# Optimization experiments

Hardware: AMD Instinct MI355X
Metric: run time of the kernel (lower is better)

The kernel has to match this reference:

```python
import jax, jax.numpy as jnp
import numpy as np

K_LAYERS = 2   # top-k layers kept in zeta routing
K_EXPERTS = 2  # top-k experts kept in alpha routing


def _topk_sparse_softmax(logits, k):
    """Keep top-k along last axis, set rest to -inf, softmax. logits [..., N]."""
    lead = logits.shape[:-1]
    n = logits.shape[-1]
    flat = logits.reshape(-1, n)
    vals, idx = jax.lax.top_k(flat, k)                      # [R,k]
    sparse = jnp.full_like(flat, -jnp.inf)
    rows = jnp.arange(flat.shape[0])[:, None]
    sparse = sparse.at[rows, idx].set(vals)
    return jax.nn.softmax(sparse, axis=-1).reshape(*lead, n)


def _lora_layer(h, W, b, A, B, zeta_l, alpha_l):
    """One backbone Linear + gated LoRA expert mixture + ReLU.
    h [B,in], W [out,in], A [E,r,in], B [E,out,r], zeta_l [B], alpha_l [B,E].
    """
    lin = h @ W.T + b                                       # [B,out]
    t = jnp.einsum('bi,eri->ber', h, A)                     # [B,E,r]
    tw = t * alpha_l[:, :, None]                            # weight experts early
    lora_sum = jnp.einsum('ber,eor->bo', tw, B)             # [B,out]
    return jax.nn.relu(lin + zeta_l[:, None] * lora_sum)


def _routing(domain_ids, dom_emb, layer_pos, Wi1, bi1, Wi2, bi2,
             Wa1, ba1, Wa2, ba2, gate_logits, R_benefit):
    M, H = dom_emb.shape
    L = layer_pos.shape[0]
    router_inp = jnp.concatenate([
        jnp.broadcast_to(dom_emb[:, None, :], (M, L, H)),
        jnp.broadcast_to(layer_pos[None, :, :], (M, L, H)),
    ], axis=-1)                                             # [M,L,2H]
    hz = jax.nn.relu(router_inp @ Wi1.T + bi1)
    zeta_logits = (hz @ Wi2.T + bi2)[..., 0]                # [M,L]
    zeta_all = _topk_sparse_softmax(zeta_logits, K_LAYERS)
    ha = jax.nn.relu(router_inp @ Wa1.T + ba1)
    alpha_logits = ha @ Wa2.T + ba2                         # [M,L,E]
    alpha_all = _topk_sparse_softmax(alpha_logits, K_EXPERTS)
    # gated benefit matrix, row-normalized
    R = jax.nn.softplus(gate_logits) * R_benefit
    R = R / jnp.clip(R.sum(-1, keepdims=True), 1e-12)
    zeta_agg = R @ zeta_all                                 # [M,L]
    alpha_agg = jnp.einsum('mn,nle->mle', R, alpha_all)     # [M,L,E]
    return zeta_agg[domain_ids], alpha_agg[domain_ids]      # [B,L],[B,L,E]


def setup_inputs() -> dict:
    key = jax.random.key(0)
    ks = jax.random.split(key, 32)
    Bsz, D0, D1, D2, D3 = 16384, 2048, 2048, 1024, 512
    E, r, M, H, L = 4, 8, 8, 64, 3
    s = 0.02
    return {
        'x': jax.random.normal(ks[0], (Bsz, D0), jnp.float32),
        'domain_ids': jax.random.randint(ks[1], (Bsz,), 0, M),
        'W1': jax.random.normal(ks[2], (D1, D0)) * s, 'b1': jnp.zeros((D1,)),
        'W2': jax.random.normal(ks[3], (D2, D1)) * s, 'b2': jnp.zeros((D2,)),
        'W3': jax.random.normal(ks[4], (D3, D2)) * s, 'b3': jnp.zeros((D3,)),
        'A1': jax.random.normal(ks[5], (E, r, D0)) * s, 'B1': jax.random.normal(ks[6], (E, D1, r)) * s,
        'A2': jax.random.normal(ks[7], (E, r, D1)) * s, 'B2': jax.random.normal(ks[8], (E, D2, r)) * s,
        'A3': jax.random.normal(ks[9], (E, r, D2)) * s, 'B3': jax.random.normal(ks[10], (E, D3, r)) * s,
        'dom_emb': jax.random.normal(ks[11], (M, H)) * s,
        'layer_pos': jax.random.normal(ks[12], (L, H)) * s,
        'Wi1': jax.random.normal(ks[13], (H, 2 * H)) * 0.1, 'bi1': jnp.zeros((H,)),
        'Wi2': jax.random.normal(ks[14], (1, H)) * 0.1, 'bi2': jnp.zeros((1,)),
        'Wa1': jax.random.normal(ks[15], (H, 2 * H)) * 0.1, 'ba1': jnp.zeros((H,)),
        'Wa2': jax.random.normal(ks[16], (E, H)) * 0.1, 'ba2': jnp.zeros((E,)),
        'gate_logits': jax.random.normal(ks[17], (M, M)) * 0.1,
        'R_benefit': jax.random.uniform(ks[18], (M, M)),
    }


def reference(x, domain_ids, W1, b1, W2, b2, W3, b3,
              A1, B1, A2, B2, A3, B3,
              dom_emb, layer_pos, Wi1, bi1, Wi2, bi2,
              Wa1, ba1, Wa2, ba2, gate_logits, R_benefit):
    zeta, alpha = _routing(domain_ids, dom_emb, layer_pos, Wi1, bi1, Wi2, bi2,
                           Wa1, ba1, Wa2, ba2, gate_logits, R_benefit)
    h = _lora_layer(x, W1, b1, A1, B1, zeta[:, 0], alpha[:, 0])
    h = _lora_layer(h, W2, b2, A2, B2, zeta[:, 1], alpha[:, 1])
    h = _lora_layer(h, W3, b3, A3, B3, zeta[:, 2], alpha[:, 2])
    return h
```

## Files before the change

### kernel.cpp

```cpp
#include <hip/hip_runtime.h>

typedef __bf16 bf16_t;
typedef __bf16 bf16x8 __attribute__((ext_vector_type(8)));
typedef __bf16 bf16x4_v __attribute__((ext_vector_type(4)));
typedef float f32x4 __attribute__((ext_vector_type(4)));

#define AS1 __attribute__((address_space(1)))
#define AS3 __attribute__((address_space(3)))

__device__ __forceinline__ void gload_lds16(const void* g, void* l) {
    __builtin_amdgcn_global_load_lds((AS1 void*)(void*)g, (AS3 void*)l, 16, 0, 0);
}

__global__ void routing_kernel(
    const float* __restrict__ dom_emb, const float* __restrict__ layer_pos,
    const float* __restrict__ Wi1, const float* __restrict__ bi1,
    const float* __restrict__ Wi2, const float* __restrict__ bi2,
    const float* __restrict__ Wa1, const float* __restrict__ ba1,
    const float* __restrict__ Wa2, const float* __restrict__ ba2,
    const float* __restrict__ gate_logits, const float* __restrict__ R_benefit,
    float* __restrict__ salpha)
{
    constexpr int M = 8, L = 3, E = 4, H = 64;
    __shared__ float zl[M * L];
    __shared__ float al[M * L][E];
    __shared__ float zeta_all[M][L];
    __shared__ float alpha_all[M][L][E];
    const int t = threadIdx.x;
    const int ml = t >> 3, js = t & 7;
    if (ml < M * L) {
        const int m = ml / L, l = ml % L;
        float zacc = 0.f;
        float aacc[E] = {0.f, 0.f, 0.f, 0.f};
        for (int jj = 0; jj < 8; ++jj) {
            const int j = js * 8 + jj;
            float hz = bi1[j], ha = ba1[j];
            for (int i = 0; i < H; ++i) {
                const float de = dom_emb[m * H + i];
                const float lp = layer_pos[l * H + i];
                hz += de * Wi1[j * 2 * H + i] + lp * Wi1[j * 2 * H + H + i];
                ha += de * Wa1[j * 2 * H + i] + lp * Wa1[j * 2 * H + H + i];
            }
            hz = fmaxf(hz, 0.f); ha = fmaxf(ha, 0.f);
            zacc += hz * Wi2[j];
            for (int e = 0; e < E; ++e) aacc[e] += ha * Wa2[e * H + j];
        }
        #pragma unroll
        for (int off = 4; off >= 1; off >>= 1) {
            zacc += __shfl_down(zacc, off, 8);
            for (int e = 0; e < E; ++e) aacc[e] += __shfl_down(aacc[e], off, 8);
        }
        if (js == 0) {
            zl[ml] = zacc + bi2[0];
            for (int e = 0; e < E; ++e) al[ml][e] = aacc[e] + ba2[e];
        }
    }
    __syncthreads();
    if (t < M) {
        const int m = t;
        float v[3] = { zl[m * L + 0], zl[m * L + 1], zl[m * L + 2] };
        int di = 0; float dv = v[0];
        for (int i = 1; i < 3; ++i) if (v[i] <= dv) { dv = v[i]; di = i; }
        float mx = -1e30f;
        for (int i = 0; i < 3; ++i) if (i != di) mx = fmaxf(mx, v[i]);
        float s = 0.f, ev[3];
        for (int i = 0; i < 3; ++i) { ev[i] = (i == di) ? 0.f : expf(v[i] - mx); s += ev[i]; }
        for (int i = 0; i < 3; ++i) zeta_all[m][i] = ev[i] / s;
        for (int l = 0; l < L; ++l) {
            float a[4];
            for (int e = 0; e < 4; ++e) a[e] = al[m * L + l][e];
            int i1 = 0;
            for (int e = 1; e < 4; ++e) if (a[e] > a[i1]) i1 = e;
            int i2 = -1;
            for (int e = 0; e < 4; ++e) { if (e == i1) continue; if (i2 < 0 || a[e] > a[i2]) i2 = e; }
            const float mx2 = fmaxf(a[i1], a[i2]);
            const float e1 = expf(a[i1] - mx2), e2 = expf(a[i2] - mx2);
            const float ss = e1 + e2;
            for (int e = 0; e < 4; ++e) alpha_all[m][l][e] = 0.f;
            alpha_all[m][l][i1] = e1 / ss;
            alpha_all[m][l][i2] = e2 / ss;
        }
    }
    __syncthreads();
    if (t < M) {
        const int m = t;
        float Rrow[8]; float rs = 0.f;
        for (int n = 0; n < M; ++n) {
            const float g = gate_logits[m * M + n];
            const float rr = log1pf(expf(g)) * R_benefit[m * M + n];
            Rrow[n] = rr; rs += rr;
        }
        rs = fmaxf(rs, 1e-12f);
        for (int l = 0; l < L; ++l) {
            float zag = 0.f, aag[4] = {0.f, 0.f, 0.f, 0.f};
            for (int n = 0; n < M; ++n) {
                const float w = Rrow[n] / rs;
                zag += w * zeta_all[n][l];
                for (int e = 0; e < 4; ++e) aag[e] += w * alpha_all[n][l][e];
            }
            for (int e = 0; e < 4; ++e) salpha[(m * L + l) * 4 + e] = zag * aag[e];
        }
    }
}

__global__ void cvt_f32_bf16(const float* __restrict__ in, bf16_t* __restrict__ out, const int n4) {
    const int i = blockIdx.x * 256 + threadIdx.x;
    if (i < n4) {
        const float4 v = ((const float4*)in)[i];
        bf16x4_v o;
        o[0] = (__bf16)v.x; o[1] = (__bf16)v.y; o[2] = (__bf16)v.z; o[3] = (__bf16)v.w;
        ((bf16x4_v*)out)[i] = o;
    }
}

__global__ void bepi_cvt(const float* __restrict__ Bsrc, bf16_t* __restrict__ out, const int Dout) {
    const int idx = blockIdx.x * 256 + threadIdx.x;
    if (idx < Dout * 32) {
        const int o = idx >> 5, c = idx & 31, e = c >> 3, r = c & 7;
        out[idx] = (__bf16)Bsrc[((size_t)e * Dout + o) * 8 + r];
    }
}

template<bool F32IN>
__global__ void __launch_bounds__(256) tw_kernel(
    const void* __restrict__ hin, bf16_t* __restrict__ xb_out,
    const bf16_t* __restrict__ Acat, const float* __restrict__ salpha,
    const int* __restrict__ dom, const int layer, const int K,
    bf16_t* __restrict__ TWb)
{
    const int t = threadIdx.x, wid = t >> 6, lane = t & 63;
    const int rb = blockIdx.x * 64 + wid * 16;
    const int ln15 = lane & 15, kg = (lane >> 4) * 8;
    const int row = rb + ln15;
    f32x4 acc0 = {0.f, 0.f, 0.f, 0.f}, acc1 = {0.f, 0.f, 0.f, 0.f};
    const bf16_t* pa0 = Acat + (size_t)ln15 * K + kg;
    const bf16_t* pa1 = pa0 + (size_t)16 * K;
    for (int k0 = 0; k0 < K; k0 += 32) {
        bf16x8 a;
        if constexpr (F32IN) {
            const float* px = (const float*)hin + (size_t)row * K + k0 + kg;
            const float4 x0 = *(const float4*)px;
            const float4 x1 = *(const float4*)(px + 4);
            a[0] = (__bf16)x0.x; a[1] = (__bf16)x0.y; a[2] = (__bf16)x0.z; a[3] = (__bf16)x0.w;
            a[4] = (__bf16)x1.x; a[5] = (__bf16)x1.y; a[6] = (__bf16)x1.z; a[7] = (__bf16)x1.w;
            *(bf16x8*)(xb_out + (size_t)row * K + k0 + kg) = a;
        } else {
            a = *(const bf16x8*)((const bf16_t*)hin + (size_t)row * K + k0 + kg);
        }
        const bf16x8 b0 = *(const bf16x8*)(pa0 + k0);
        const bf16x8 b1 = *(const bf16x8*)(pa1 + k0);
        acc0 = __builtin_amdgcn_mfma_f32_16x16x32_bf16(a, b0, acc0, 0, 0, 0);
        acc1 = __builtin_amdgcn_mfma_f32_16x16x32_bf16(a, b1, acc1, 0, 0, 0);
    }
    const int rbase = rb + (lane >> 4) * 4;
    #pragma unroll
    for (int i = 0; i < 4; ++i) {
        const int r2 = rbase + i;
        const int d = dom[r2];
        const float* sa = salpha + (d * 3 + layer) * 4;
        const float s0 = sa[ln15 >> 3];
        const float s1 = sa[2 + (ln15 >> 3)];
        TWb[(size_t)r2 * 32 + ln15]      = (__bf16)(acc0[i] * s0);
        TWb[(size_t)r2 * 32 + 16 + ln15] = (__bf16)(acc1[i] * s1);
    }
}


__device__ __forceinline__ void stage_chunk64(const bf16_t* g, int ldK, char* chunk, int t) {
    #pragma unroll
    for (int w = 0; w < 2; ++w) {
        const int row = t >> 2;
        const int sl = t & 3;
        const int src = sl ^ (((row >> 3) & 1) << 1);
        gload_lds16(g + (size_t)row * ldK + w * 32 + src * 8, chunk + w * 8192 + t * 16);
    }
}

__device__ __forceinline__ void stage_chunk32(const bf16_t* g, char* chunk, int t) {
    const int row = t >> 2;
    const int sl = t & 3;
    const int src = sl ^ (((row >> 3) & 1) << 1);
    gload_lds16(g + (size_t)row * 32 + src * 8, chunk + t * 16);
}

__global__ void __launch_bounds__(512, 2) gemm_lora8(
    const bf16_t* __restrict__ Abuf, const bf16_t* __restrict__ Wbuf,
    const float* __restrict__ bias, const bf16_t* __restrict__ TWb,
    const bf16_t* __restrict__ Bepi, bf16_t* __restrict__ outp,
    const int N, const int K, const int nwg_n)
{
    __shared__ __align__(1024) char lds[131072];
    const int t = threadIdx.x;
    const int wid = t >> 6, lane = t & 63;
    const int wm = wid >> 2, wn = wid & 3, wnh = wn >> 1;
    const int cpx = gridDim.x >> 3;
    const int wg = (blockIdx.x & 7) * cpx + (blockIdx.x >> 3);
    const int row0 = (wg / nwg_n) * 256, col0 = (wg % nwg_n) * 256;

    const int r15 = lane & 15;
    const int swb = ((lane >> 4) ^ (((lane >> 3) & 1) << 1)) << 4;

    auto achunk = [&](int p, int c) -> char* { return lds + (((p << 1) + c) << 14); };
    auto bchunk = [&](int p, int c) -> char* { return lds + 65536 + (((p << 1) + c) << 14); };

    const bf16_t* Ab = Abuf + (size_t)row0 * K;
    const bf16_t* Bb = Wbuf + (size_t)col0 * K;
    const size_t halfA = (size_t)128 * K;

    f32x4 acc[8][4] = {};
    bf16x8 aF[4], bF[4];

    auto readA = [&](char* c, int mbase, int kq) {
        #pragma unroll
        for (int i = 0; i < 4; ++i)
            aF[i] = *(const bf16x8*)(c + (kq << 13) + (((mbase + i) * 16 + r15) << 6) + swb);
    };
    auto readB = [&](char* c, int kq) {
        #pragma unroll
        for (int nf = 0; nf < 4; ++nf)
            bF[nf] = *(const bf16x8*)(c + (kq << 13) + (((wn & 1) * 64 + nf * 16 + r15) << 6) + swb);
    };
    auto mfma16 = [&](int mbase) {
        __builtin_amdgcn_s_setprio(1);
        #pragma unroll
        for (int mf = 0; mf < 4; ++mf)
            #pragma unroll
            for (int nf = 0; nf < 4; ++nf)
                acc[mbase + mf][nf] =
                    __builtin_amdgcn_mfma_f32_16x16x32_bf16(aF[mf], bF[nf], acc[mbase + mf][nf], 0, 0, 0);
        __builtin_amdgcn_s_setprio(0);
    };
    #define MIDSYNC() do { __builtin_amdgcn_s_barrier(); \
        asm volatile("s_waitcnt lgkmcnt(0)" ::: "memory"); \
        __builtin_amdgcn_sched_barrier(0); } while (0)
    #define ENDBAR() __builtin_amdgcn_s_barrier()

    const int NT = K >> 6;

    stage_chunk64(Ab,               K, achunk(0, 0), t);
    stage_chunk64(Ab + halfA,       K, achunk(0, 1), t);
    stage_chunk64(Bb,               K, bchunk(0, 0), t);
    stage_chunk64(Bb + halfA,       K, bchunk(0, 1), t);
    stage_chunk64(Bb + 64,          K, bchunk(1, 0), t);
    stage_chunk64(Bb + halfA + 64,  K, bchunk(1, 1), t);
    asm volatile("s_waitcnt vmcnt(4)" ::: "memory");
    __builtin_amdgcn_s_barrier();

    for (int T = 0; T < NT; ++T) {
        const int p = T & 1, q = p ^ 1;
        const size_t ko1 = (size_t)(T + 1) << 6, ko2 = (size_t)(T + 2) << 6;
        char* myA = achunk(p, wm);
        char* myB = bchunk(p, wnh);
        if (T + 1 < NT) stage_chunk64(Ab + ko1, K, achunk(q, 0), t);
        readA(myA, 0, 0);
        readB(myB, 0);
        if (T == NT - 1) asm volatile("s_waitcnt vmcnt(0)" ::: "memory");
        MIDSYNC();
        mfma16(0);
        ENDBAR();
        if (T + 1 < NT) stage_chunk64(Ab + halfA + ko1, K, achunk(q, 1), t);
        readA(myA, 4, 0);
        MIDSYNC();
        mfma16(4);
        ENDBAR();
        readA(myA, 4, 1);
        readB(myB, 1);
        MIDSYNC();
        mfma16(4);
        ENDBAR();
        if (T + 2 < NT) {
            stage_chunk64(Bb + ko2,         K, bchunk(p, 0), t);
            stage_chunk64(Bb + halfA + ko2, K, bchunk(p, 1), t);
        }
        readA(myA, 0, 1);
        asm volatile("s_waitcnt vmcnt(4)" ::: "memory");
        MIDSYNC();
        mfma16(0);
        ENDBAR();
    }

    {
        const int q2 = NT & 1;
        stage_chunk32(TWb + (size_t)row0 * 32,          achunk(q2, 0), t);
        stage_chunk32(TWb + (size_t)(row0 + 128) * 32,  achunk(q2, 1), t);
        stage_chunk32(Bepi + (size_t)col0 * 32,         bchunk(q2, 0), t);
        stage_chunk32(Bepi + (size_t)(col0 + 128) * 32, bchunk(q2, 1), t);
        asm volatile("s_waitcnt vmcnt(0)" ::: "memory");
        __builtin_amdgcn_s_barrier();
        char* lA_ = achunk(q2, wm);
        char* lB_ = bchunk(q2, wnh);
        #pragma unroll
        for (int nf = 0; nf < 4; ++nf)
            bF[nf] = *(const bf16x8*)(lB_ + (((wn & 1) * 64 + nf * 16 + r15) << 6) + swb);
        #pragma unroll
        for (int i = 0; i < 4; ++i)
            aF[i] = *(const bf16x8*)(lA_ + ((i * 16 + r15) << 6) + swb);
        asm volatile("s_waitcnt lgkmcnt(0)" ::: "memory");
        __builtin_amdgcn_sched_barrier(0);
        mfma16(0);
        #pragma unroll
        for (int i = 0; i < 4; ++i)
            aF[i] = *(const bf16x8*)(lA_ + (((i + 4) * 16 + r15) << 6) + swb);
        asm volatile("s_waitcnt lgkmcnt(0)" ::: "memory");
        __builtin_amdgcn_sched_barrier(0);
        mfma16(4);
    }

    const int orow = row0 + wm * 128 + (lane >> 4) * 4;
    const int ocol = col0 + wn * 64 + r15;
    #pragma unroll
    for (int nf = 0; nf < 4; ++nf) {
        const int col = ocol + nf * 16;
        const float bn = bias[col];
        #pragma unroll
        for (int mf = 0; mf < 8; ++mf) {
            const int rbase = orow + mf * 16;
            #pragma unroll
            for (int i = 0; i < 4; ++i) {
                const float v = fmaxf(acc[mf][nf][i] + bn, 0.f);
                outp[(size_t)(rbase + i) * N + col] = (__bf16)v;
            }
        }
    }
    #undef MIDSYNC
    #undef ENDBAR
}

#define BM 128
#define BN 128
#define BK 32

template<bool OUT_F32>
__global__ void __launch_bounds__(256) gemm_lora(
    const bf16_t* __restrict__ Abuf, const bf16_t* __restrict__ Wbuf,
    const float* __restrict__ bias, const bf16_t* __restrict__ TWb,
    const bf16_t* __restrict__ Bepi, void* __restrict__ outp,
    const int N, const int K)
{
    __shared__ bf16_t lA[BM * BK];
    __shared__ bf16_t lB[BN * BK];
    const int t = threadIdx.x;
    const int row0 = blockIdx.y * BM;
    const int col0 = blockIdx.x * BN;
    const int wid = t >> 6, lane = t & 63;
    const int wr = wid >> 1, wc = wid & 1;
    const int ln15 = lane & 15, kg = (lane >> 4) * 8;
    const int srow = t >> 2, sg8 = (t & 3) * 8;
    const bf16_t* gA = Abuf + (size_t)(row0 + srow) * K + sg8;
    const bf16_t* gB = Wbuf + (size_t)(col0 + srow) * K + sg8;
    bf16_t* ldA  = &lA[t * 8];
    bf16_t* ldA2 = &lA[2048 + t * 8];
    bf16_t* ldB  = &lB[t * 8];
    bf16_t* ldB2 = &lB[2048 + t * 8];
    f32x4 acc[4][4] = {};
    const int aoff = (wr * 64 + ln15) * BK + kg;
    const int boff = (wc * 64 + ln15) * BK + kg;

    auto compute_tile = [&]() {
        bf16x8 af[4], bfr[4];
        #pragma unroll
        for (int m = 0; m < 4; ++m) af[m] = *(const bf16x8*)&lA[aoff + m * 16 * BK];
        #pragma unroll
        for (int n = 0; n < 4; ++n) bfr[n] = *(const bf16x8*)&lB[boff + n * 16 * BK];
        #pragma unroll
        for (int m = 0; m < 4; ++m)
            #pragma unroll
            for (int n = 0; n < 4; ++n)
                acc[m][n] = __builtin_amdgcn_mfma_f32_16x16x32_bf16(af[m], bfr[n], acc[m][n], 0, 0, 0);
    };

    const size_t half = (size_t)64 * K;
    const int nk = K / BK;
    for (int kt = 0; kt < nk; ++kt) {
        gload_lds16(gA + kt * BK, ldA);
        gload_lds16(gA + half + kt * BK, ldA2);
        gload_lds16(gB + kt * BK, ldB);
        gload_lds16(gB + half + kt * BK, ldB2);
        __syncthreads();
        compute_tile();
        __syncthreads();
    }
    gload_lds16(TWb + (size_t)(row0 + srow) * 32 + sg8, ldA);
    gload_lds16(TWb + (size_t)(row0 + 64 + srow) * 32 + sg8, ldA2);
    gload_lds16(Bepi + (size_t)(col0 + srow) * 32 + sg8, ldB);
    gload_lds16(Bepi + (size_t)(col0 + 64 + srow) * 32 + sg8, ldB2);
    __syncthreads();
    compute_tile();

    const int orow = row0 + wr * 64 + (lane >> 4) * 4;
    const int ocol = col0 + wc * 64 + ln15;
    #pragma unroll
    for (int n = 0; n < 4; ++n) {
        const int col = ocol + n * 16;
        const float bn = bias[col];
        #pragma unroll
        for (int m = 0; m < 4; ++m) {
            const int rbase = orow + m * 16;
            #pragma unroll
            for (int i = 0; i < 4; ++i) {
                const float v = fmaxf(acc[m][n][i] + bn, 0.f);
                if constexpr (OUT_F32)
                    ((float*)outp)[(size_t)(rbase + i) * N + col] = v;
                else
                    ((bf16_t*)outp)[(size_t)(rbase + i) * N + col] = (__bf16)v;
            }
        }
    }
}

extern "C" void kernel_launch(void* const* d_in, const int* in_sizes, int n_in,
                              void* d_out, int out_size, void* d_ws, size_t ws_size,
                              hipStream_t stream)
{
    const float* x    = (const float*)d_in[0];
    const int*   dom  = (const int*)d_in[1];
    const float* W1   = (const float*)d_in[2];  const float* b1  = (const float*)d_in[3];
    const float* W2   = (const float*)d_in[4];  const float* b2  = (const float*)d_in[5];
    const float* W3   = (const float*)d_in[6];  const float* b3  = (const float*)d_in[7];
    const float* A1   = (const float*)d_in[8];  const float* B1  = (const float*)d_in[9];
    const float* A2   = (const float*)d_in[10]; const float* B2  = (const float*)d_in[11];
    const float* A3   = (const float*)d_in[12]; const float* B3  = (const float*)d_in[13];
    const float* dome = (const float*)d_in[14]; const float* lpos = (const float*)d_in[15];
    const float* Wi1  = (const float*)d_in[16]; const float* bi1 = (const float*)d_in[17];
    const float* Wi2  = (const float*)d_in[18]; const float* bi2 = (const float*)d_in[19];
    const float* Wa1  = (const float*)d_in[20]; const float* ba1 = (const float*)d_in[21];
    const float* Wa2  = (const float*)d_in[22]; const float* ba2 = (const float*)d_in[23];
    const float* gate = (const float*)d_in[24]; const float* Rb  = (const float*)d_in[25];
    (void)in_sizes; (void)n_in; (void)out_size; (void)ws_size;

    constexpr int Bsz = 16384, D0 = 2048, D1 = 2048, D2 = 1024, D3 = 512;

    char* ws = (char*)d_ws;
    size_t off = 0;
    auto alloc = [&](size_t bytes) -> void* {
        void* p = ws + off;
        off = (off + bytes + 255) & ~(size_t)255;
        return p;
    };
    float*  salpha = (float*) alloc(8 * 3 * 4 * sizeof(float));
    bf16_t* W1b = (bf16_t*)alloc((size_t)D1 * D0 * 2);
    bf16_t* W2b = (bf16_t*)alloc((size_t)D2 * D1 * 2);
    bf16_t* W3b = (bf16_t*)alloc((size_t)D3 * D2 * 2);
    bf16_t* Ac1 = (bf16_t*)alloc((size_t)32 * D0 * 2);
    bf16_t* Ac2 = (bf16_t*)alloc((size_t)32 * D1 * 2);
    bf16_t* Ac3 = (bf16_t*)alloc((size_t)32 * D2 * 2);
    bf16_t* Be1 = (bf16_t*)alloc((size_t)D1 * 32 * 2);
    bf16_t* Be2 = (bf16_t*)alloc((size_t)D2 * 32 * 2);
    bf16_t* Be3 = (bf16_t*)alloc((size_t)D3 * 32 * 2);
    bf16_t* TWb = (bf16_t*)alloc((size_t)Bsz * 32 * 2);
    bf16_t* xb  = (bf16_t*)alloc((size_t)Bsz * D0 * 2);
    bf16_t* h1b = (bf16_t*)alloc((size_t)Bsz * D1 * 2);
    bf16_t* h2b = xb;

    routing_kernel<<<1, 256, 0, stream>>>(dome, lpos, Wi1, bi1, Wi2, bi2,
                                          Wa1, ba1, Wa2, ba2, gate, Rb, salpha);

    cvt_f32_bf16<<<(D1 * D0 / 4 + 255) / 256, 256, 0, stream>>>(W1, W1b, D1 * D0 / 4);
    cvt_f32_bf16<<<(D2 * D1 / 4 + 255) / 256, 256, 0, stream>>>(W2, W2b, D2 * D1 / 4);
    cvt_f32_bf16<<<(D3 * D2 / 4 + 255) / 256, 256, 0, stream>>>(W3, W3b, D3 * D2 / 4);
    cvt_f32_bf16<<<(32 * D0 / 4 + 255) / 256, 256, 0, stream>>>(A1, Ac1, 32 * D0 / 4);
    cvt_f32_bf16<<<(32 * D1 / 4 + 255) / 256, 256, 0, stream>>>(A2, Ac2, 32 * D1 / 4);
    cvt_f32_bf16<<<(32 * D2 / 4 + 255) / 256, 256, 0, stream>>>(A3, Ac3, 32 * D2 / 4);
    bepi_cvt<<<(D1 * 32 + 255) / 256, 256, 0, stream>>>(B1, Be1, D1);
    bepi_cvt<<<(D2 * 32 + 255) / 256, 256, 0, stream>>>(B2, Be2, D2);
    bepi_cvt<<<(D3 * 32 + 255) / 256, 256, 0, stream>>>(B3, Be3, D3);

    tw_kernel<true><<<Bsz / 64, 256, 0, stream>>>(x, xb, Ac1, salpha, dom, 0, D0, TWb);
    gemm_lora8<<<(Bsz / 256) * (D1 / 256), 512, 0, stream>>>(xb, W1b, b1, TWb, Be1, h1b, D1, D0, D1 / 256);
    tw_kernel<false><<<Bsz / 64, 256, 0, stream>>>(h1b, nullptr, Ac2, salpha, dom, 1, D1, TWb);
    gemm_lora8<<<(Bsz / 256) * (D2 / 256), 512, 0, stream>>>(h1b, W2b, b2, TWb, Be2, h2b, D2, D1, D2 / 256);
    tw_kernel<false><<<Bsz / 64, 256, 0, stream>>>(h2b, nullptr, Ac3, salpha, dom, 2, D2, TWb);
    gemm_lora<true><<<dim3(D3 / BN, Bsz / BM), 256, 0, stream>>>(h2b, W3b, b3, TWb, Be3, d_out, D3, D2);
}
```

Measured before the change: 418.3 us.

## Interleave GEMM tile prefetch per phase and fuse weight conversion launches

The main GEMM's global-to-LDS staging is reorganized. Instead of loading whole 64-wide A and B chunks at a few points, with B prefetched two tiles ahead, it now issues half-chunk loads for the next tile spread across the four MFMA phases. It uses precomputed per-thread source pointers and tuned vmcnt waits, so load issue should overlap compute more evenly with less address arithmetic. Separately, the nine small f32-to-bf16 conversion launches are merged into two kernels that write one contiguous destination. That merge assumes the bf16 buffers are allocated back-to-back and hardcodes the problem sizes.

```diff
diff --git a/kernel.cpp b/kernel.cpp
--- a/kernel.cpp
+++ b/kernel.cpp
@@ -103,22 +103,44 @@
     }
 }
 
-__global__ void cvt_f32_bf16(const float* __restrict__ in, bf16_t* __restrict__ out, const int n4) {
+__global__ void cvt_fused(const float* __restrict__ s0, const float* __restrict__ s1,
+                          const float* __restrict__ s2, const float* __restrict__ s3,
+                          const float* __restrict__ s4, const float* __restrict__ s5,
+                          bf16_t* __restrict__ dst)
+{
     const int i = blockIdx.x * 256 + threadIdx.x;
-    if (i < n4) {
-        const float4 v = ((const float4*)in)[i];
-        bf16x4_v o;
-        o[0] = (__bf16)v.x; o[1] = (__bf16)v.y; o[2] = (__bf16)v.z; o[3] = (__bf16)v.w;
-        ((bf16x4_v*)out)[i] = o;
-    }
-}
-
-__global__ void bepi_cvt(const float* __restrict__ Bsrc, bf16_t* __restrict__ out, const int Dout) {
+    constexpr int b0 = 1048576;
+    constexpr int b1 = b0 + 524288;
+    constexpr int b2 = b1 + 131072;
+    constexpr int b3 = b2 + 16384;
+    constexpr int b4 = b3 + 16384;
+    constexpr int b5 = b4 + 8192;
+    if (i >= b5) return;
+    const float* src; int rel;
+    if (i < b0)      { src = s0; rel = i; }
+    else if (i < b1) { src = s1; rel = i - b0; }
+    else if (i < b2) { src = s2; rel = i - b1; }
+    else if (i < b3) { src = s3; rel = i - b2; }
+    else if (i < b4) { src = s4; rel = i - b3; }
+    else             { src = s5; rel = i - b4; }
+    const float4 v = ((const float4*)src)[rel];
+    bf16x4_v o;
+    o[0] = (__bf16)v.x; o[1] = (__bf16)v.y; o[2] = (__bf16)v.z; o[3] = (__bf16)v.w;
+    ((bf16x4_v*)dst)[i] = o;
+}
+
+__global__ void bepi_fused(const float* __restrict__ B1, const float* __restrict__ B2,
+                           const float* __restrict__ B3, bf16_t* __restrict__ dst)
+{
     const int idx = blockIdx.x * 256 + threadIdx.x;
-    if (idx < Dout * 32) {
-        const int o = idx >> 5, c = idx & 31, e = c >> 3, r = c & 7;
-        out[idx] = (__bf16)Bsrc[((size_t)e * Dout + o) * 8 + r];
-    }
+    constexpr int c1 = 2048 * 32, c2 = c1 + 1024 * 32, c3 = c2 + 512 * 32;
+    if (idx >= c3) return;
+    const float* B; int rel, Dout;
+    if (idx < c1)      { B = B1; rel = idx;      Dout = 2048; }
+    else if (idx < c2) { B = B2; rel = idx - c1; Dout = 1024; }
+    else               { B = B3; rel = idx - c2; Dout = 512; }
+    const int o = rel >> 5, c = rel & 31, e = c >> 3, r = c & 7;
+    dst[idx] = (__bf16)B[((size_t)e * Dout + o) * 8 + r];
 }
 
 template<bool F32IN>
@@ -166,16 +188,6 @@
 }
 
 
-__device__ __forceinline__ void stage_chunk64(const bf16_t* g, int ldK, char* chunk, int t) {
-    #pragma unroll
-    for (int w = 0; w < 2; ++w) {
-        const int row = t >> 2;
-        const int sl = t & 3;
-        const int src = sl ^ (((row >> 3) & 1) << 1);
-        gload_lds16(g + (size_t)row * ldK + w * 32 + src * 8, chunk + w * 8192 + t * 16);
-    }
-}
-
 __device__ __forceinline__ void stage_chunk32(const bf16_t* g, char* chunk, int t) {
     const int row = t >> 2;
     const int sl = t & 3;
@@ -203,9 +215,12 @@
     auto achunk = [&](int p, int c) -> char* { return lds + (((p << 1) + c) << 14); };
     auto bchunk = [&](int p, int c) -> char* { return lds + 65536 + (((p << 1) + c) << 14); };
 
-    const bf16_t* Ab = Abuf + (size_t)row0 * K;
-    const bf16_t* Bb = Wbuf + (size_t)col0 * K;
+    const int srow = t >> 2, ssl = t & 3;
+    const int ssrc = ssl ^ (((srow >> 3) & 1) << 1);
+    const bf16_t* sA = Abuf + (size_t)(row0 + srow) * K + ssrc * 8;
+    const bf16_t* sB = Wbuf + (size_t)(col0 + srow) * K + ssrc * 8;
     const size_t halfA = (size_t)128 * K;
+    const int dt16 = t * 16;
 
     f32x4 acc[8][4] = {};
     bf16x8 aF[4], bF[4];
@@ -237,46 +252,58 @@
 
     const int NT = K >> 6;
 
-    stage_chunk64(Ab,               K, achunk(0, 0), t);
-    stage_chunk64(Ab + halfA,       K, achunk(0, 1), t);
-    stage_chunk64(Bb,               K, bchunk(0, 0), t);
-    stage_chunk64(Bb + halfA,       K, bchunk(0, 1), t);
-    stage_chunk64(Bb + 64,          K, bchunk(1, 0), t);
-    stage_chunk64(Bb + halfA + 64,  K, bchunk(1, 1), t);
+    gload_lds16(sA,              lds + 0     + dt16);
+    gload_lds16(sA + halfA,      lds + 16384 + dt16);
+    gload_lds16(sB,              lds + 65536 + dt16);
+    gload_lds16(sB + halfA,      lds + 81920 + dt16);
+    gload_lds16(sA + 32,         lds + 8192  + dt16);
+    gload_lds16(sA + halfA + 32, lds + 24576 + dt16);
+    gload_lds16(sB + 32,         lds + 73728 + dt16);
+    gload_lds16(sB + halfA + 32, lds + 90112 + dt16);
     asm volatile("s_waitcnt vmcnt(4)" ::: "memory");
     __builtin_amdgcn_s_barrier();
 
+    const bf16_t* pA = sA + 64;
+    const bf16_t* pB = sB + 64;
+
     for (int T = 0; T < NT; ++T) {
         const int p = T & 1, q = p ^ 1;
-        const size_t ko1 = (size_t)(T + 1) << 6, ko2 = (size_t)(T + 2) << 6;
         char* myA = achunk(p, wm);
         char* myB = bchunk(p, wnh);
-        if (T + 1 < NT) stage_chunk64(Ab + ko1, K, achunk(q, 0), t);
+        char* dA = lds + (q << 15) + dt16;
+        char* dB = lds + 65536 + (q << 15) + dt16;
+        const bool more = (T < NT - 1);
         readA(myA, 0, 0);
         readB(myB, 0);
-        if (T == NT - 1) asm volatile("s_waitcnt vmcnt(0)" ::: "memory");
+        if (more) { gload_lds16(pA, dA); gload_lds16(pA + halfA, dA + 16384); }
         MIDSYNC();
         mfma16(0);
         ENDBAR();
-        if (T + 1 < NT) stage_chunk64(Ab + halfA + ko1, K, achunk(q, 1), t);
         readA(myA, 4, 0);
+        if (more) {
+            gload_lds16(pB, dB); gload_lds16(pB + halfA, dB + 16384);
+            asm volatile("s_waitcnt vmcnt(4)" ::: "memory");
+        } else {
+            asm volatile("s_waitcnt vmcnt(0)" ::: "memory");
+        }
         MIDSYNC();
         mfma16(4);
         ENDBAR();
         readA(myA, 4, 1);
         readB(myB, 1);
+        if (more) { gload_lds16(pA + 32, dA + 8192); gload_lds16(pA + halfA + 32, dA + 24576); }
         MIDSYNC();
         mfma16(4);
         ENDBAR();
-        if (T + 2 < NT) {
-            stage_chunk64(Bb + ko2,         K, bchunk(p, 0), t);
-            stage_chunk64(Bb + halfA + ko2, K, bchunk(p, 1), t);
-        }
         readA(myA, 0, 1);
-        asm volatile("s_waitcnt vmcnt(4)" ::: "memory");
+        if (more) {
+            gload_lds16(pB + 32, dB + 8192); gload_lds16(pB + halfA + 32, dB + 24576);
+            asm volatile("s_waitcnt vmcnt(4)" ::: "memory");
+        }
         MIDSYNC();
         mfma16(0);
         ENDBAR();
+        pA += 64; pB += 64;
     }
 
     {
@@ -455,15 +482,8 @@
     routing_kernel<<<1, 256, 0, stream>>>(dome, lpos, Wi1, bi1, Wi2, bi2,
                                           Wa1, ba1, Wa2, ba2, gate, Rb, salpha);
 
-    cvt_f32_bf16<<<(D1 * D0 / 4 + 255) / 256, 256, 0, stream>>>(W1, W1b, D1 * D0 / 4);
-    cvt_f32_bf16<<<(D2 * D1 / 4 + 255) / 256, 256, 0, stream>>>(W2, W2b, D2 * D1 / 4);
-    cvt_f32_bf16<<<(D3 * D2 / 4 + 255) / 256, 256, 0, stream>>>(W3, W3b, D3 * D2 / 4);
-    cvt_f32_bf16<<<(32 * D0 / 4 + 255) / 256, 256, 0, stream>>>(A1, Ac1, 32 * D0 / 4);
-    cvt_f32_bf16<<<(32 * D1 / 4 + 255) / 256, 256, 0, stream>>>(A2, Ac2, 32 * D1 / 4);
-    cvt_f32_bf16<<<(32 * D2 / 4 + 255) / 256, 256, 0, stream>>>(A3, Ac3, 32 * D2 / 4);
-    bepi_cvt<<<(D1 * 32 + 255) / 256, 256, 0, stream>>>(B1, Be1, D1);
-    bepi_cvt<<<(D2 * 32 + 255) / 256, 256, 0, stream>>>(B2, Be2, D2);
-    bepi_cvt<<<(D3 * 32 + 255) / 256, 256, 0, stream>>>(B3, Be3, D3);
+    cvt_fused<<<6816, 256, 0, stream>>>(W1, W2, W3, A1, A2, A3, W1b);
+    bepi_fused<<<448, 256, 0, stream>>>(B1, B2, B3, Be1);
 
     tw_kernel<true><<<Bsz / 64, 256, 0, stream>>>(x, xb, Ac1, salpha, dom, 0, D0, TWb);
     gemm_lora8<<<(Bsz / 256) * (D1 / 256), 512, 0, stream>>>(xb, W1b, b1, TWb, Be1, h1b, D1, D0, D1 / 256);
```

New measurement: 416.5 us. About the same (-0.4%).
